# Kernel tuning notes

Hardware: AMD Instinct MI355X
Metric: run time of the kernel (lower is better)

## Reference

```python
import jax, jax.numpy as jnp
import numpy as np

T, B, Q, H = 100, 256, 2048, 1024  # steps, students, n_questions, n_hidden
NIN = 2 * Q                         # n_input = 2 * n_questions


def setup_inputs() -> dict:
    key = jax.random.key(0)
    ks = jax.random.split(key, 8)
    s = 0.02  # init scale
    return {
        "x_idx": jax.random.randint(ks[0], (T, B), 0, NIN),          # one-hot index into 2Q
        "y_idx": jax.random.randint(ks[1], (T, B), 0, Q),             # next-question one-hot index
        "truth": (jax.random.uniform(ks[2], (T, B)) > 0.5).astype(jnp.float32),
        "Wm": jax.random.normal(ks[3], (H, H), jnp.float32) * s,
        "bm": jnp.zeros((H,), jnp.float32),
        "Wx": jax.random.normal(ks[4], (H, NIN), jnp.float32) * s,
        "bx": jnp.zeros((H,), jnp.float32),
        "Wy": jax.random.normal(ks[5], (Q, H), jnp.float32) * s,
        "by": jnp.zeros((Q,), jnp.float32),
        "W_start": jax.random.normal(ks[6], (H, 1), jnp.float32) * s,
        "b_start": jnp.zeros((H,), jnp.float32),
    }


def reference(x_idx, y_idx, truth, Wm, bm, Wx, bx, Wy, by, W_start, b_start):
    # state = start(zeros(B,1)): zeros @ W_start^T + b_start -> [B, H]
    h0 = jnp.zeros((B, 1), Wm.dtype) @ W_start.T + b_start

    # lin_x(input_x) with one-hot input_x == column-select of Wx: [T, B, H]
    xproj = Wx.T[x_idx] + bx

    def step(h, xp):
        h = jnp.tanh(h @ Wm.T + bm + xp)  # Elman cell: tanh(lin_m(h) + lin_x(x))
        return h, h

    _, hiddens = jax.lax.scan(step, h0, xproj)  # hiddens: [T, B, H]

    # pred = sum(sigmoid(lin_y(h)) * y_onehot) == sigmoid(logit at y_idx)
    Wy_sel = Wy[y_idx]                                        # [T, B, H]
    logits = jnp.einsum('tbh,tbh->tb', hiddens, Wy_sel) + by[y_idx]
    pred = jax.nn.sigmoid(logits)                             # [T, B]

    # BCELoss(reduction='none'): -(t*log(p) + (1-t)*log(1-p)); stable via log_sigmoid
    loss = -(truth * jax.nn.log_sigmoid(logits) + (1.0 - truth) * jax.nn.log_sigmoid(-logits))
    return pred, loss
```

## Files before the change

kernel.cpp:

```cpp
#include <hip/hip_runtime.h>
#include <hip/hip_bf16.h>
#include <math.h>

#define T_STEPS 100
#define B 256
#define Q 2048
#define H 1024
#define NIN 4096

typedef __attribute__((ext_vector_type(8))) short bf16x8;
typedef __attribute__((ext_vector_type(4))) short bf16x4;
typedef __attribute__((ext_vector_type(4))) float f32x4;
typedef __attribute__((ext_vector_type(4))) unsigned u32x4;
typedef unsigned long long u64;

#define HLDS0_OFF 0
#define HLDS1_OFF 16384
#define HOUT_OFF  32768
#define LOGIT_OFF (32768 + 2048)
#define SMEM_BYTES (LOGIT_OFF + 256)

#define H0_OFF 0
#define H1_OFF (512 * 1024)
#define LP_OFF (1024 * 1024)
#define FLAG_OFF (LP_OFF + 1638400)

#define AGENT __HIP_MEMORY_SCOPE_AGENT

__device__ inline unsigned short f2bf(float f) {
    union { float f; unsigned int u; } c; c.f = f;
    unsigned int u = c.u + 0x7fffu + ((c.u >> 16) & 1u);
    return (unsigned short)(u >> 16);
}

__device__ __forceinline__ unsigned bytes_ge(unsigned w, unsigned f) {
    return ((w & 0xffu) >= f) & (((w >> 8) & 0xffu) >= f) &
           (((w >> 16) & 0xffu) >= f) & (((w >> 24) & 0xffu) >= f);
}

__device__ __forceinline__ void sg_bar_bytes(unsigned char* fb, int rg, unsigned fval) {
    asm volatile("s_waitcnt vmcnt(0)" ::: "memory");
    __syncthreads();
    if (threadIdx.x == 0) {
        asm volatile("global_store_byte %0, %1, off sc0 sc1"
                     :: "v"(fb + rg), "v"(fval) : "memory");
        u32x4 fw;
        unsigned done;
        do {
            asm volatile("global_load_dwordx4 %0, %1, off sc0 sc1"
                         : "=v"(fw) : "v"(fb));
            asm volatile("s_waitcnt vmcnt(0)" ::: "memory");
            done = bytes_ge(fw[0], fval) & bytes_ge(fw[1], fval) &
                   bytes_ge(fw[2], fval) & bytes_ge(fw[3], fval);
        } while (!done);
    }
    __syncthreads();
}

__global__ void ws_init(unsigned* __restrict__ flags) {
    int idx = blockIdx.x * blockDim.x + threadIdx.x;
    if (idx < 16 * 16) flags[idx] = 0u;
}

__global__ __launch_bounds__(256, 1) void rnn_persistent(
    const int* __restrict__ x_idx, const int* __restrict__ y_idx,
    const float* __restrict__ truth,
    const float* __restrict__ Wm, const float* __restrict__ bm,
    const float* __restrict__ Wx, const float* __restrict__ bx_,
    const float* __restrict__ Wy, const float* __restrict__ by,
    const float* __restrict__ b_start,
    __hip_bfloat16* __restrict__ h0buf, __hip_bfloat16* __restrict__ h1buf,
    float* __restrict__ lp, unsigned* __restrict__ flags,
    float* __restrict__ out)
{
    extern __shared__ char lds[];

    const int tid = threadIdx.x;
    const int bid = blockIdx.x;
    const int rg = bid & 15;
    const int sg = bid >> 4;
    const int sbase = sg * 16;
    const int w  = tid >> 6;
    const int l  = tid & 63;
    const int lr = l & 15;
    const int g  = l >> 4;

    unsigned char* fb = (unsigned char*)(flags + sg * 16);

    bf16x8 a_frag[32];
    {
        const int row = rg * 64 + w * 16 + lr;
        const float* wrow = &Wm[(size_t)row * H];
        #pragma unroll
        for (int half = 0; half < 2; ++half) {
            #pragma unroll
            for (int kk = 0; kk < 16; ++kk) {
                int k0 = (half * 64 + kk * 4 + g) * 8;
                float4 v0 = *reinterpret_cast<const float4*>(&wrow[k0]);
                float4 v1 = *reinterpret_cast<const float4*>(&wrow[k0 + 4]);
                bf16x8 f;
                f[0] = (short)f2bf(v0.x); f[1] = (short)f2bf(v0.y);
                f[2] = (short)f2bf(v0.z); f[3] = (short)f2bf(v0.w);
                f[4] = (short)f2bf(v1.x); f[5] = (short)f2bf(v1.y);
                f[6] = (short)f2bf(v1.z); f[7] = (short)f2bf(v1.w);
                a_frag[half * 16 + kk] = f;
            }
        }
    }
    {
        int s = tid >> 4, c8 = tid & 15;
        union { unsigned short s4[4]; u64 u; } pk;
        #pragma unroll
        for (int e = 0; e < 4; ++e) pk.s4[e] = f2bf(b_start[rg * 64 + c8 * 4 + e]);
        __hip_atomic_store((u64*)&h0buf[(size_t)(sbase + s) * H + rg * 64 + c8 * 4],
                           pk.u, __ATOMIC_RELAXED, AGENT);
    }
    float bias_r[4];
    #pragma unroll
    for (int r = 0; r < 4; ++r) {
        int gi = rg * 64 + w * 16 + g * 4 + r;
        bias_r[r] = bm[gi] + bx_[gi];
    }
    float wx_r[4], wy_r[4];
    {
        int xc = x_idx[sbase + lr];
        int yc = y_idx[sbase + lr];
        #pragma unroll
        for (int r = 0; r < 4; ++r) {
            int gi = rg * 64 + w * 16 + g * 4 + r;
            wx_r[r] = Wx[(size_t)gi * NIN + xc];
            wy_r[r] = Wy[(size_t)yc * H + gi];
        }
    }

    sg_bar_bytes(fb, rg, 1u);

    for (int t = 0; t < T_STEPS; ++t) {
        const __hip_bfloat16* hc = (t & 1) ? h1buf : h0buf;
        __hip_bfloat16*       hn = (t & 1) ? h0buf : h1buf;

        bf16x8 hv0[4], hv1[4];
        #pragma unroll
        for (int it = 0; it < 4; ++it) {
            int q = it * 256 + tid;
            int srow = q >> 6, sl = q & 63;
            const __hip_bfloat16* p = &hc[(size_t)(sbase + srow) * H + sl * 8];
            asm volatile("global_load_dwordx4 %0, %1, off sc0 sc1"
                         : "=v"(hv0[it]) : "v"(p));
        }
        #pragma unroll
        for (int it = 0; it < 4; ++it) {
            int q = it * 256 + tid;
            int srow = q >> 6, sl = q & 63;
            const __hip_bfloat16* p = &hc[(size_t)(sbase + srow) * H + 512 + sl * 8];
            asm volatile("global_load_dwordx4 %0, %1, off sc0 sc1"
                         : "=v"(hv1[it]) : "v"(p));
        }
        asm volatile("s_waitcnt vmcnt(0)" ::: "memory");
        __builtin_amdgcn_sched_barrier(0);

        #pragma unroll
        for (int it = 0; it < 4; ++it) {
            int q = it * 256 + tid;
            int srow = q >> 6, sl = q & 63;
            *reinterpret_cast<bf16x8*>(
                &lds[HLDS0_OFF + srow * 1024 + ((sl ^ (srow & 7)) << 4)]) = hv0[it];
        }
        #pragma unroll
        for (int it = 0; it < 4; ++it) {
            int q = it * 256 + tid;
            int srow = q >> 6, sl = q & 63;
            *reinterpret_cast<bf16x8*>(
                &lds[HLDS1_OFF + srow * 1024 + ((sl ^ (srow & 7)) << 4)]) = hv1[it];
        }
        __syncthreads();

        f32x4 acc0 = {0.f, 0.f, 0.f, 0.f};
        f32x4 acc1 = {0.f, 0.f, 0.f, 0.f};
        #pragma unroll
        for (int kk = 0; kk < 16; kk += 2) {
            bf16x8 b0 = *reinterpret_cast<const bf16x8*>(
                &lds[HLDS0_OFF + lr * 1024 + ((((kk    ) * 4 + g) ^ (lr & 7)) << 4)]);
            acc0 = __builtin_amdgcn_mfma_f32_16x16x32_bf16(a_frag[kk],     b0, acc0, 0, 0, 0);
            bf16x8 b1 = *reinterpret_cast<const bf16x8*>(
                &lds[HLDS0_OFF + lr * 1024 + ((((kk + 1) * 4 + g) ^ (lr & 7)) << 4)]);
            acc1 = __builtin_amdgcn_mfma_f32_16x16x32_bf16(a_frag[kk + 1], b1, acc1, 0, 0, 0);
        }
        #pragma unroll
        for (int kk = 0; kk < 16; kk += 2) {
            bf16x8 b0 = *reinterpret_cast<const bf16x8*>(
                &lds[HLDS1_OFF + lr * 1024 + ((((kk    ) * 4 + g) ^ (lr & 7)) << 4)]);
            acc0 = __builtin_amdgcn_mfma_f32_16x16x32_bf16(a_frag[16 + kk],     b0, acc0, 0, 0, 0);
            bf16x8 b1 = *reinterpret_cast<const bf16x8*>(
                &lds[HLDS1_OFF + lr * 1024 + ((((kk + 1) * 4 + g) ^ (lr & 7)) << 4)]);
            acc1 = __builtin_amdgcn_mfma_f32_16x16x32_bf16(a_frag[16 + kk + 1], b1, acc1, 0, 0, 0);
        }

        float hv[4];
        #pragma unroll
        for (int r = 0; r < 4; ++r)
            hv[r] = tanhf(acc0[r] + acc1[r] + bias_r[r] + wx_r[r]);

        {
            int row0  = w * 16 + g * 4;
            int chunk = row0 >> 3;
            bf16x4 b4;
            b4[0] = (short)f2bf(hv[0]); b4[1] = (short)f2bf(hv[1]);
            b4[2] = (short)f2bf(hv[2]); b4[3] = (short)f2bf(hv[3]);
            int byte = HOUT_OFF + lr * 128 + ((chunk ^ (lr & 7)) << 4) + ((row0 & 7) << 1);
            *reinterpret_cast<bf16x4*>(&lds[byte]) = b4;
        }
        {
            float p = hv[0] * wy_r[0] + hv[1] * wy_r[1] + hv[2] * wy_r[2] + hv[3] * wy_r[3];
            p += __shfl_down(p, 32);
            p += __shfl_down(p, 16);
            if (l < 16)
                *reinterpret_cast<float*>(&lds[LOGIT_OFF + (w * 16 + l) * 4]) = p;
        }
        __syncthreads();
        if (tid < 128) {
            int s = tid >> 3, c16 = tid & 7;
            bf16x8 v = *reinterpret_cast<const bf16x8*>(
                &lds[HOUT_OFF + s * 128 + ((c16 ^ (s & 7)) << 4)]);
            const __hip_bfloat16* dst = &hn[(size_t)(sbase + s) * H + rg * 64 + c16 * 8];
            asm volatile("global_store_dwordx4 %0, %1, off sc0 sc1"
                         :: "v"(dst), "v"(v) : "memory");
        }
        if (tid < 16) {
            const float* lg = reinterpret_cast<const float*>(&lds[LOGIT_OFF]);
            float ps = lg[tid] + lg[16 + tid] + lg[32 + tid] + lg[48 + tid];
            __hip_atomic_store(&lp[(size_t)(t * 16 + rg) * B + sbase + tid],
                               ps, __ATOMIC_RELAXED, AGENT);
        }

        {
            const unsigned fval = (unsigned)(t + 2);
            asm volatile("s_waitcnt vmcnt(0)" ::: "memory");
            __syncthreads();
            if (tid == 0)
                asm volatile("global_store_byte %0, %1, off sc0 sc1"
                             :: "v"(fb + rg), "v"(fval) : "memory");

            {
                int tn = (t + 1 < T_STEPS) ? t + 1 : t;
                int xc = x_idx[tn * B + sbase + lr];
                int yc = y_idx[tn * B + sbase + lr];
                #pragma unroll
                for (int r = 0; r < 4; ++r) {
                    int gi = rg * 64 + w * 16 + g * 4 + r;
                    wx_r[r] = Wx[(size_t)gi * NIN + xc];
                    wy_r[r] = Wy[(size_t)yc * H + gi];
                }
            }

            if (tid == 0) {
                u32x4 fw;
                unsigned done;
                do {
                    asm volatile("global_load_dwordx4 %0, %1, off sc0 sc1"
                                 : "=v"(fw) : "v"(fb));
                    asm volatile("s_waitcnt vmcnt(0)" ::: "memory");
                    done = bytes_ge(fw[0], fval) & bytes_ge(fw[1], fval) &
                           bytes_ge(fw[2], fval) & bytes_ge(fw[3], fval);
                } while (!done);
            }
            __syncthreads();
        }
    }

    {
        int ti = tid >> 4, s = tid & 15;
        int t = rg + ti * 16;
        if (t < T_STEPS) {
            int idx = t * B + sbase + s;
            float lgv = 0.f;
            #pragma unroll
            for (int rgi = 0; rgi < 16; ++rgi)
                lgv += __hip_atomic_load(&lp[(size_t)(t * 16 + rgi) * B + sbase + s],
                                         __ATOMIC_RELAXED, AGENT);
            int yc = y_idx[idx];
            lgv += by[yc];
            float pred = 1.f / (1.f + expf(-lgv));
            float tv = truth[idx];
            float e = log1pf(expf(-fabsf(lgv)));
            float ls_pos = fminf(lgv, 0.f) - e;
            float ls_neg = fminf(-lgv, 0.f) - e;
            out[idx] = pred;
            out[T_STEPS * B + idx] = -(tv * ls_pos + (1.f - tv) * ls_neg);
        }
    }
}

extern "C" void kernel_launch(void* const* d_in, const int* in_sizes, int n_in,
                              void* d_out, int out_size, void* d_ws, size_t ws_size,
                              hipStream_t stream) {
    const int*   x_idx   = (const int*)d_in[0];
    const int*   y_idx   = (const int*)d_in[1];
    const float* truth   = (const float*)d_in[2];
    const float* Wm      = (const float*)d_in[3];
    const float* bm      = (const float*)d_in[4];
    const float* Wx      = (const float*)d_in[5];
    const float* bx_     = (const float*)d_in[6];
    const float* Wy      = (const float*)d_in[7];
    const float* by      = (const float*)d_in[8];
    const float* b_start = (const float*)d_in[10];
    float* out = (float*)d_out;

    __hip_bfloat16* h0buf = (__hip_bfloat16*)((char*)d_ws + H0_OFF);
    __hip_bfloat16* h1buf = (__hip_bfloat16*)((char*)d_ws + H1_OFF);
    float*          lp    = (float*)((char*)d_ws + LP_OFF);
    unsigned*       flags = (unsigned*)((char*)d_ws + FLAG_OFF);

    ws_init<<<1, 256, 0, stream>>>(flags);

    rnn_persistent<<<dim3(256), dim3(256), SMEM_BYTES, stream>>>(
        x_idx, y_idx, truth, Wm, bm, Wx, bx_, Wy, by, b_start,
        h0buf, h1buf, lp, flags, out);
}
```

Before: 429.5 us.

## Process two student groups per block, halving grid to 128 persistent blocks

Each persistent block now handles 32 students (two 16-student tiles) against the same register-resident Wm slice, so the grid shrinks from 256 to 128 blocks. Each block does twice the MFMA work and twice the hidden-state traffic per step, while the per-step barrier among the 16 blocks of a group is kept. The hidden-state loads and stores switch from dwordx4 asm with sc0/sc1 to relaxed 64-bit atomics. The aim is fewer blocks and barrier participants per step, at the cost of longer per-step critical paths on half as many CUs.

```diff
diff --git a/kernel.cpp b/kernel.cpp
--- a/kernel.cpp
+++ b/kernel.cpp
@@ -14,11 +14,15 @@
 typedef __attribute__((ext_vector_type(4))) unsigned u32x4;
 typedef unsigned long long u64;
 
-#define HLDS0_OFF 0
-#define HLDS1_OFF 16384
-#define HOUT_OFF  32768
-#define LOGIT_OFF (32768 + 2048)
-#define SMEM_BYTES (LOGIT_OFF + 256)
+#define HLDS_A0 0
+#define HLDS_A1 16384
+#define HLDS_B0 32768
+#define HLDS_B1 49152
+#define HOUT_A  65536
+#define HOUT_B  67584
+#define LOGIT_A 69632
+#define LOGIT_B 69888
+#define SMEM_BYTES 70144
 
 #define H0_OFF 0
 #define H1_OFF (512 * 1024)
@@ -38,7 +42,7 @@
            (((w >> 16) & 0xffu) >= f) & (((w >> 24) & 0xffu) >= f);
 }
 
-__device__ __forceinline__ void sg_bar_bytes(unsigned char* fb, int rg, unsigned fval) {
+__device__ __forceinline__ void sgp_bar(unsigned char* fb, int rg, unsigned fval) {
     asm volatile("s_waitcnt vmcnt(0)" ::: "memory");
     __syncthreads();
     if (threadIdx.x == 0) {
@@ -59,7 +63,7 @@
 
 __global__ void ws_init(unsigned* __restrict__ flags) {
     int idx = blockIdx.x * blockDim.x + threadIdx.x;
-    if (idx < 16 * 16) flags[idx] = 0u;
+    if (idx < 128) flags[idx] = 0u;
 }
 
 __global__ __launch_bounds__(256, 1) void rnn_persistent(
@@ -77,15 +81,15 @@
 
     const int tid = threadIdx.x;
     const int bid = blockIdx.x;
-    const int rg = bid & 15;
-    const int sg = bid >> 4;
-    const int sbase = sg * 16;
+    const int rg  = bid & 15;
+    const int sgp = bid >> 4;
+    const int sbase = sgp * 32;
     const int w  = tid >> 6;
     const int l  = tid & 63;
     const int lr = l & 15;
     const int g  = l >> 4;
 
-    unsigned char* fb = (unsigned char*)(flags + sg * 16);
+    unsigned char* fb = (unsigned char*)flags + sgp * 64;
 
     bf16x8 a_frag[32];
     {
@@ -108,12 +112,16 @@
         }
     }
     {
-        int s = tid >> 4, c8 = tid & 15;
-        union { unsigned short s4[4]; u64 u; } pk;
-        #pragma unroll
-        for (int e = 0; e < 4; ++e) pk.s4[e] = f2bf(b_start[rg * 64 + c8 * 4 + e]);
-        __hip_atomic_store((u64*)&h0buf[(size_t)(sbase + s) * H + rg * 64 + c8 * 4],
-                           pk.u, __ATOMIC_RELAXED, AGENT);
+        int s = tid >> 3, c = tid & 7;
+        union { unsigned short s4[4]; u64 u; } pk0, pk1;
+        #pragma unroll
+        for (int e = 0; e < 4; ++e) {
+            pk0.s4[e] = f2bf(b_start[rg * 64 + c * 8 + e]);
+            pk1.s4[e] = f2bf(b_start[rg * 64 + c * 8 + 4 + e]);
+        }
+        u64* dst = (u64*)&h0buf[(size_t)(sbase + s) * H + rg * 64 + c * 8];
+        __hip_atomic_store(dst,     pk0.u, __ATOMIC_RELAXED, AGENT);
+        __hip_atomic_store(dst + 1, pk1.u, __ATOMIC_RELAXED, AGENT);
     }
     float bias_r[4];
     #pragma unroll
@@ -121,155 +129,177 @@
         int gi = rg * 64 + w * 16 + g * 4 + r;
         bias_r[r] = bm[gi] + bx_[gi];
     }
-    float wx_r[4], wy_r[4];
+    float wxA[4], wyA[4], wxB[4], wyB[4];
     {
-        int xc = x_idx[sbase + lr];
-        int yc = y_idx[sbase + lr];
+        int xcA = x_idx[sbase + lr],      ycA = y_idx[sbase + lr];
+        int xcB = x_idx[sbase + 16 + lr], ycB = y_idx[sbase + 16 + lr];
         #pragma unroll
         for (int r = 0; r < 4; ++r) {
             int gi = rg * 64 + w * 16 + g * 4 + r;
-            wx_r[r] = Wx[(size_t)gi * NIN + xc];
-            wy_r[r] = Wy[(size_t)yc * H + gi];
-        }
-    }
-
-    sg_bar_bytes(fb, rg, 1u);
+            wxA[r] = Wx[(size_t)gi * NIN + xcA];
+            wyA[r] = Wy[(size_t)ycA * H + gi];
+            wxB[r] = Wx[(size_t)gi * NIN + xcB];
+            wyB[r] = Wy[(size_t)ycB * H + gi];
+        }
+    }
+
+    sgp_bar(fb, rg, 1u);
 
     for (int t = 0; t < T_STEPS; ++t) {
         const __hip_bfloat16* hc = (t & 1) ? h1buf : h0buf;
         __hip_bfloat16*       hn = (t & 1) ? h0buf : h1buf;
 
-        bf16x8 hv0[4], hv1[4];
+        u64 rA[16], rB[16];
         #pragma unroll
         for (int it = 0; it < 4; ++it) {
             int q = it * 256 + tid;
             int srow = q >> 6, sl = q & 63;
-            const __hip_bfloat16* p = &hc[(size_t)(sbase + srow) * H + sl * 8];
-            asm volatile("global_load_dwordx4 %0, %1, off sc0 sc1"
-                         : "=v"(hv0[it]) : "v"(p));
-        }
+            const u64* sA0 = (const u64*)&hc[(size_t)(sbase + srow) * H + sl * 8];
+            const u64* sA1 = (const u64*)&hc[(size_t)(sbase + srow) * H + 512 + sl * 8];
+            const u64* sB0 = (const u64*)&hc[(size_t)(sbase + 16 + srow) * H + sl * 8];
+            const u64* sB1 = (const u64*)&hc[(size_t)(sbase + 16 + srow) * H + 512 + sl * 8];
+            rA[2 * it]         = __hip_atomic_load(sA0,     __ATOMIC_RELAXED, AGENT);
+            rA[2 * it + 1]     = __hip_atomic_load(sA0 + 1, __ATOMIC_RELAXED, AGENT);
+            rA[8 + 2 * it]     = __hip_atomic_load(sA1,     __ATOMIC_RELAXED, AGENT);
+            rA[8 + 2 * it + 1] = __hip_atomic_load(sA1 + 1, __ATOMIC_RELAXED, AGENT);
+            rB[2 * it]         = __hip_atomic_load(sB0,     __ATOMIC_RELAXED, AGENT);
+            rB[2 * it + 1]     = __hip_atomic_load(sB0 + 1, __ATOMIC_RELAXED, AGENT);
+            rB[8 + 2 * it]     = __hip_atomic_load(sB1,     __ATOMIC_RELAXED, AGENT);
+            rB[8 + 2 * it + 1] = __hip_atomic_load(sB1 + 1, __ATOMIC_RELAXED, AGENT);
+        }
+
         #pragma unroll
         for (int it = 0; it < 4; ++it) {
             int q = it * 256 + tid;
             int srow = q >> 6, sl = q & 63;
-            const __hip_bfloat16* p = &hc[(size_t)(sbase + srow) * H + 512 + sl * 8];
-            asm volatile("global_load_dwordx4 %0, %1, off sc0 sc1"
-                         : "=v"(hv1[it]) : "v"(p));
-        }
-        asm volatile("s_waitcnt vmcnt(0)" ::: "memory");
-        __builtin_amdgcn_sched_barrier(0);
-
-        #pragma unroll
-        for (int it = 0; it < 4; ++it) {
-            int q = it * 256 + tid;
-            int srow = q >> 6, sl = q & 63;
-            *reinterpret_cast<bf16x8*>(
-                &lds[HLDS0_OFF + srow * 1024 + ((sl ^ (srow & 7)) << 4)]) = hv0[it];
-        }
-        #pragma unroll
-        for (int it = 0; it < 4; ++it) {
-            int q = it * 256 + tid;
-            int srow = q >> 6, sl = q & 63;
-            *reinterpret_cast<bf16x8*>(
-                &lds[HLDS1_OFF + srow * 1024 + ((sl ^ (srow & 7)) << 4)]) = hv1[it];
+            int so = srow * 1024 + ((sl ^ (srow & 7)) << 4);
+            union { u64 u[2]; bf16x8 v; } cA0, cA1, cB0, cB1;
+            cA0.u[0] = rA[2 * it];     cA0.u[1] = rA[2 * it + 1];
+            cA1.u[0] = rA[8 + 2 * it]; cA1.u[1] = rA[8 + 2 * it + 1];
+            cB0.u[0] = rB[2 * it];     cB0.u[1] = rB[2 * it + 1];
+            cB1.u[0] = rB[8 + 2 * it]; cB1.u[1] = rB[8 + 2 * it + 1];
+            *reinterpret_cast<bf16x8*>(&lds[HLDS_A0 + so]) = cA0.v;
+            *reinterpret_cast<bf16x8*>(&lds[HLDS_A1 + so]) = cA1.v;
+            *reinterpret_cast<bf16x8*>(&lds[HLDS_B0 + so]) = cB0.v;
+            *reinterpret_cast<bf16x8*>(&lds[HLDS_B1 + so]) = cB1.v;
         }
         __syncthreads();
 
-        f32x4 acc0 = {0.f, 0.f, 0.f, 0.f};
-        f32x4 acc1 = {0.f, 0.f, 0.f, 0.f};
+        f32x4 aA0 = {0.f,0.f,0.f,0.f}, aA1 = {0.f,0.f,0.f,0.f};
         #pragma unroll
         for (int kk = 0; kk < 16; kk += 2) {
             bf16x8 b0 = *reinterpret_cast<const bf16x8*>(
-                &lds[HLDS0_OFF + lr * 1024 + ((((kk    ) * 4 + g) ^ (lr & 7)) << 4)]);
-            acc0 = __builtin_amdgcn_mfma_f32_16x16x32_bf16(a_frag[kk],     b0, acc0, 0, 0, 0);
+                &lds[HLDS_A0 + lr * 1024 + ((((kk    ) * 4 + g) ^ (lr & 7)) << 4)]);
+            aA0 = __builtin_amdgcn_mfma_f32_16x16x32_bf16(a_frag[kk],     b0, aA0, 0, 0, 0);
             bf16x8 b1 = *reinterpret_cast<const bf16x8*>(
-                &lds[HLDS0_OFF + lr * 1024 + ((((kk + 1) * 4 + g) ^ (lr & 7)) << 4)]);
-            acc1 = __builtin_amdgcn_mfma_f32_16x16x32_bf16(a_frag[kk + 1], b1, acc1, 0, 0, 0);
+                &lds[HLDS_A0 + lr * 1024 + ((((kk + 1) * 4 + g) ^ (lr & 7)) << 4)]);
+            aA1 = __builtin_amdgcn_mfma_f32_16x16x32_bf16(a_frag[kk + 1], b1, aA1, 0, 0, 0);
         }
         #pragma unroll
         for (int kk = 0; kk < 16; kk += 2) {
             bf16x8 b0 = *reinterpret_cast<const bf16x8*>(
-                &lds[HLDS1_OFF + lr * 1024 + ((((kk    ) * 4 + g) ^ (lr & 7)) << 4)]);
-            acc0 = __builtin_amdgcn_mfma_f32_16x16x32_bf16(a_frag[16 + kk],     b0, acc0, 0, 0, 0);
+                &lds[HLDS_A1 + lr * 1024 + ((((kk    ) * 4 + g) ^ (lr & 7)) << 4)]);
+            aA0 = __builtin_amdgcn_mfma_f32_16x16x32_bf16(a_frag[16 + kk],     b0, aA0, 0, 0, 0);
             bf16x8 b1 = *reinterpret_cast<const bf16x8*>(
-                &lds[HLDS1_OFF + lr * 1024 + ((((kk + 1) * 4 + g) ^ (lr & 7)) << 4)]);
-            acc1 = __builtin_amdgcn_mfma_f32_16x16x32_bf16(a_frag[16 + kk + 1], b1, acc1, 0, 0, 0);
-        }
-
-        float hv[4];
-        #pragma unroll
-        for (int r = 0; r < 4; ++r)
-            hv[r] = tanhf(acc0[r] + acc1[r] + bias_r[r] + wx_r[r]);
+                &lds[HLDS_A1 + lr * 1024 + ((((kk + 1) * 4 + g) ^ (lr & 7)) << 4)]);
+            aA1 = __builtin_amdgcn_mfma_f32_16x16x32_bf16(a_frag[16 + kk + 1], b1, aA1, 0, 0, 0);
+        }
+        f32x4 aB0 = {0.f,0.f,0.f,0.f}, aB1 = {0.f,0.f,0.f,0.f};
+        #pragma unroll
+        for (int kk = 0; kk < 16; kk += 2) {
+            bf16x8 b0 = *reinterpret_cast<const bf16x8*>(
+                &lds[HLDS_B0 + lr * 1024 + ((((kk    ) * 4 + g) ^ (lr & 7)) << 4)]);
+            aB0 = __builtin_amdgcn_mfma_f32_16x16x32_bf16(a_frag[kk],     b0, aB0, 0, 0, 0);
+            bf16x8 b1 = *reinterpret_cast<const bf16x8*>(
+                &lds[HLDS_B0 + lr * 1024 + ((((kk + 1) * 4 + g) ^ (lr & 7)) << 4)]);
+            aB1 = __builtin_amdgcn_mfma_f32_16x16x32_bf16(a_frag[kk + 1], b1, aB1, 0, 0, 0);
+        }
+        #pragma unroll
+        for (int kk = 0; kk < 16; kk += 2) {
+            bf16x8 b0 = *reinterpret_cast<const bf16x8*>(
+                &lds[HLDS_B1 + lr * 1024 + ((((kk    ) * 4 + g) ^ (lr & 7)) << 4)]);
+            aB0 = __builtin_amdgcn_mfma_f32_16x16x32_bf16(a_frag[16 + kk],     b0, aB0, 0, 0, 0);
+            bf16x8 b1 = *reinterpret_cast<const bf16x8*>(
+                &lds[HLDS_B1 + lr * 1024 + ((((kk + 1) * 4 + g) ^ (lr & 7)) << 4)]);
+            aB1 = __builtin_amdgcn_mfma_f32_16x16x32_bf16(a_frag[16 + kk + 1], b1, aB1, 0, 0, 0);
+        }
 
         {
-            int row0  = w * 16 + g * 4;
-            int chunk = row0 >> 3;
+            float hvo[4];
+            #pragma unroll
+            for (int r = 0; r < 4; ++r)
+                hvo[r] = tanhf(aA0[r] + aA1[r] + bias_r[r] + wxA[r]);
+            int row0 = w * 16 + g * 4, chunk = row0 >> 3;
             bf16x4 b4;
-            b4[0] = (short)f2bf(hv[0]); b4[1] = (short)f2bf(hv[1]);
-            b4[2] = (short)f2bf(hv[2]); b4[3] = (short)f2bf(hv[3]);
-            int byte = HOUT_OFF + lr * 128 + ((chunk ^ (lr & 7)) << 4) + ((row0 & 7) << 1);
-            *reinterpret_cast<bf16x4*>(&lds[byte]) = b4;
-        }
-        {
-            float p = hv[0] * wy_r[0] + hv[1] * wy_r[1] + hv[2] * wy_r[2] + hv[3] * wy_r[3];
+            b4[0] = (short)f2bf(hvo[0]); b4[1] = (short)f2bf(hvo[1]);
+            b4[2] = (short)f2bf(hvo[2]); b4[3] = (short)f2bf(hvo[3]);
+            *reinterpret_cast<bf16x4*>(
+                &lds[HOUT_A + lr * 128 + ((chunk ^ (lr & 7)) << 4) + ((row0 & 7) << 1)]) = b4;
+            float p = hvo[0] * wyA[0] + hvo[1] * wyA[1] + hvo[2] * wyA[2] + hvo[3] * wyA[3];
             p += __shfl_down(p, 32);
             p += __shfl_down(p, 16);
             if (l < 16)
-                *reinterpret_cast<float*>(&lds[LOGIT_OFF + (w * 16 + l) * 4]) = p;
+                *reinterpret_cast<float*>(&lds[LOGIT_A + (w * 16 + l) * 4]) = p;
+        }
+        {
+            float hvo[4];
+            #pragma unroll
+            for (int r = 0; r < 4; ++r)
+                hvo[r] = tanhf(aB0[r] + aB1[r] + bias_r[r] + wxB[r]);
+            int row0 = w * 16 + g * 4, chunk = row0 >> 3;
+            bf16x4 b4;
+            b4[0] = (short)f2bf(hvo[0]); b4[1] = (short)f2bf(hvo[1]);
+            b4[2] = (short)f2bf(hvo[2]); b4[3] = (short)f2bf(hvo[3]);
+            *reinterpret_cast<bf16x4*>(
+                &lds[HOUT_B + lr * 128 + ((chunk ^ (lr & 7)) << 4) + ((row0 & 7) << 1)]) = b4;
+            float p = hvo[0] * wyB[0] + hvo[1] * wyB[1] + hvo[2] * wyB[2] + hvo[3] * wyB[3];
+            p += __shfl_down(p, 32);
+            p += __shfl_down(p, 16);
+            if (l < 16)
+                *reinterpret_cast<float*>(&lds[LOGIT_B + (w * 16 + l) * 4]) = p;
         }
         __syncthreads();
-        if (tid < 128) {
-            int s = tid >> 3, c16 = tid & 7;
-            bf16x8 v = *reinterpret_cast<const bf16x8*>(
-                &lds[HOUT_OFF + s * 128 + ((c16 ^ (s & 7)) << 4)]);
-            const __hip_bfloat16* dst = &hn[(size_t)(sbase + s) * H + rg * 64 + c16 * 8];
-            asm volatile("global_store_dwordx4 %0, %1, off sc0 sc1"
-                         :: "v"(dst), "v"(v) : "memory");
+
+        {
+            int s = tid >> 4, c8 = tid & 15;
+            int lo = s * 128 + (((c8 >> 1) ^ (s & 7)) << 4) + ((c8 & 1) << 3);
+            u64 vA = *reinterpret_cast<const u64*>(&lds[HOUT_A + lo]);
+            u64 vB = *reinterpret_cast<const u64*>(&lds[HOUT_B + lo]);
+            __hip_atomic_store((u64*)&hn[(size_t)(sbase + s) * H + rg * 64 + c8 * 4],
+                               vA, __ATOMIC_RELAXED, AGENT);
+            __hip_atomic_store((u64*)&hn[(size_t)(sbase + 16 + s) * H + rg * 64 + c8 * 4],
+                               vB, __ATOMIC_RELAXED, AGENT);
         }
         if (tid < 16) {
-            const float* lg = reinterpret_cast<const float*>(&lds[LOGIT_OFF]);
-            float ps = lg[tid] + lg[16 + tid] + lg[32 + tid] + lg[48 + tid];
+            const float* lgA = reinterpret_cast<const float*>(&lds[LOGIT_A]);
+            const float* lgB = reinterpret_cast<const float*>(&lds[LOGIT_B]);
+            float psA = lgA[tid] + lgA[16 + tid] + lgA[32 + tid] + lgA[48 + tid];
+            float psB = lgB[tid] + lgB[16 + tid] + lgB[32 + tid] + lgB[48 + tid];
             __hip_atomic_store(&lp[(size_t)(t * 16 + rg) * B + sbase + tid],
-                               ps, __ATOMIC_RELAXED, AGENT);
+                               psA, __ATOMIC_RELAXED, AGENT);
+            __hip_atomic_store(&lp[(size_t)(t * 16 + rg) * B + sbase + 16 + tid],
+                               psB, __ATOMIC_RELAXED, AGENT);
         }
 
         {
-            const unsigned fval = (unsigned)(t + 2);
-            asm volatile("s_waitcnt vmcnt(0)" ::: "memory");
-            __syncthreads();
-            if (tid == 0)
-                asm volatile("global_store_byte %0, %1, off sc0 sc1"
-                             :: "v"(fb + rg), "v"(fval) : "memory");
-
-            {
-                int tn = (t + 1 < T_STEPS) ? t + 1 : t;
-                int xc = x_idx[tn * B + sbase + lr];
-                int yc = y_idx[tn * B + sbase + lr];
-                #pragma unroll
-                for (int r = 0; r < 4; ++r) {
-                    int gi = rg * 64 + w * 16 + g * 4 + r;
-                    wx_r[r] = Wx[(size_t)gi * NIN + xc];
-                    wy_r[r] = Wy[(size_t)yc * H + gi];
-                }
+            int tn = (t + 1 < T_STEPS) ? t + 1 : t;
+            int xcA = x_idx[tn * B + sbase + lr],      ycA = y_idx[tn * B + sbase + lr];
+            int xcB = x_idx[tn * B + sbase + 16 + lr], ycB = y_idx[tn * B + sbase + 16 + lr];
+            #pragma unroll
+            for (int r = 0; r < 4; ++r) {
+                int gi = rg * 64 + w * 16 + g * 4 + r;
+                wxA[r] = Wx[(size_t)gi * NIN + xcA];
+                wyA[r] = Wy[(size_t)ycA * H + gi];
+                wxB[r] = Wx[(size_t)gi * NIN + xcB];
+                wyB[r] = Wy[(size_t)ycB * H + gi];
             }
-
-            if (tid == 0) {
-                u32x4 fw;
-                unsigned done;
-                do {
-                    asm volatile("global_load_dwordx4 %0, %1, off sc0 sc1"
-                                 : "=v"(fw) : "v"(fb));
-                    asm volatile("s_waitcnt vmcnt(0)" ::: "memory");
-                    done = bytes_ge(fw[0], fval) & bytes_ge(fw[1], fval) &
-                           bytes_ge(fw[2], fval) & bytes_ge(fw[3], fval);
-                } while (!done);
-            }
-            __syncthreads();
-        }
+        }
+
+        sgp_bar(fb, rg, (unsigned)(t + 2));
     }
 
     {
-        int ti = tid >> 4, s = tid & 15;
+        int ti = tid >> 5, s = tid & 31;
         int t = rg + ti * 16;
         if (t < T_STEPS) {
             int idx = t * B + sbase + s;
@@ -313,7 +343,10 @@
 
     ws_init<<<1, 256, 0, stream>>>(flags);
 
-    rnn_persistent<<<dim3(256), dim3(256), SMEM_BYTES, stream>>>(
+    hipFuncSetAttribute(reinterpret_cast<const void*>(rnn_persistent),
+                        hipFuncAttributeMaxDynamicSharedMemorySize, SMEM_BYTES);
+
+    rnn_persistent<<<dim3(128), dim3(256), SMEM_BYTES, stream>>>(
         x_idx, y_idx, truth, Wm, bm, Wx, bx_, Wy, by, b_start,
         h0buf, h1buf, lp, flags, out);
 }
```

Result: slower. 697.5 us (+62.4%).
